# Kernel optimization log

Hardware: AMD Instinct MI355X
Metric: run time of the kernel (lower is better)

## Reference

```python
import jax, jax.numpy as jnp
import numpy as np

B, L, C = 8, 2000, 256
PATCH_LIST = [10, 20]


def _interp_linear(z, L_out):
    # z: (B, L_in, C) -> (B, L_out, C); torch F.interpolate mode='linear', align_corners=False
    L_in = z.shape[1]
    pos = (jnp.arange(L_out, dtype=jnp.float32) + 0.5) * (L_in / L_out) - 0.5
    pos = jnp.clip(pos, 0.0, L_in - 1.0)
    lo = jnp.floor(pos).astype(jnp.int32)
    hi = jnp.minimum(lo + 1, L_in - 1)
    frac = (pos - lo.astype(jnp.float32))[None, :, None]
    return z[:, lo, :] * (1.0 - frac) + z[:, hi, :] * frac


def _kaiming(key, out_dim, in_dim):
    # kaiming_normal_ mode='fan_out', nonlinearity='relu': std = sqrt(2/fan_out)
    return jax.random.normal(key, (out_dim, in_dim), jnp.float32) * np.float32(np.sqrt(2.0 / out_dim))


def setup_inputs() -> dict:
    key = jax.random.key(0)
    ks = jax.random.split(key, 7)
    inp = {"x": jax.random.normal(ks[0], (B, L, C), jnp.float32)}
    ki = 1
    for p in PATCH_LIST:
        w = L // p  # patch_number
        inp[f"wq{p}"] = _kaiming(ks[ki], p, p); ki += 1
        inp[f"bq{p}"] = jnp.zeros((p,), jnp.float32)
        inp[f"wk{p}"] = _kaiming(ks[ki], p, p); ki += 1
        inp[f"bk{p}"] = jnp.zeros((p,), jnp.float32)
        inp[f"wl{p}"] = _kaiming(ks[ki], w, p); ki += 1  # nn.Linear(patch_size, patch_number)
        inp[f"bl{p}"] = jnp.zeros((w,), jnp.float32)
    return inp


def _scale_branch(x, p, wq, bq, wk, bk, wl, bl):
    Bx, Lx, Cx = x.shape
    w = Lx // p
    # rearrange 'b (w p) c -> (b c) w p'
    z = x.reshape(Bx, w, p, Cx).transpose(0, 3, 1, 2).reshape(Bx * Cx, w, p)
    # AttentionLayer(w_size=w, d_model=p, n_heads=1): attn map over the w patches
    q = z @ wq.T + bq
    k = z @ wk.T + bk
    scores = jnp.einsum('nwp,nvp->nwv', q, k) / jnp.sqrt(jnp.float32(p))  # (B*C, w, w)
    attn = jax.nn.softmax(scores, axis=-1)
    # linear_layers[i]: Linear(p -> w); attention OUTPUT is discarded in the original forward
    z2 = z @ wl.T + bl  # (B*C, w, w)
    # rearrange '(b c) w p2 -> b (w p2) c'
    z3 = z2.reshape(Bx, Cx, w * w).transpose(0, 2, 1)  # (B, w*w, C)
    if w * w != Lx:
        z3 = _interp_linear(z3, Lx)
    return z3, attn


def reference(x, wq10, bq10, wk10, bk10, wl10, bl10, wq20, bq20, wk20, bk20, wl20, bl20):
    z10, attn10 = _scale_branch(x, 10, wq10, bq10, wk10, bk10, wl10, bl10)
    z20, attn20 = _scale_branch(x, 20, wq20, bq20, wk20, bk20, wl20, bl20)
    res = (z10 + z20) * 0.5  # stack(...).mean(-1) over the two scales
    return res, attn10, attn20
```

## Files before the change

### kernel.cpp

```cpp
#include <hip/hip_runtime.h>
#include <cstddef>
#include <cstdint>

#define XSTRIDE 512000
#define RES_ELEMS 4096000
#define ATTN10_ELEMS 81920000

typedef _Float16 half2_t __attribute__((ext_vector_type(2)));

__device__ __forceinline__ unsigned int pack_h2(float a, float b) {
  half2_t h;
  h.x = (_Float16)a;
  h.y = (_Float16)b;
  return __builtin_bit_cast(unsigned int, h);
}

__device__ __forceinline__ float fdot2(unsigned int a, unsigned int b, float c) {
#if __has_builtin(__builtin_amdgcn_fdot2)
  return __builtin_amdgcn_fdot2(__builtin_bit_cast(half2_t, a),
                                __builtin_bit_cast(half2_t, b), c, false);
#else
  half2_t ha = __builtin_bit_cast(half2_t, a);
  half2_t hb = __builtin_bit_cast(half2_t, b);
  return c + (float)ha.x * (float)hb.x + (float)ha.y * (float)hb.y;
#endif
}

template <int CTRL>
__device__ __forceinline__ float dpp_f(float x, float identity) {
  return __int_as_float(__builtin_amdgcn_update_dpp(
      __float_as_int(identity), __float_as_int(x), CTRL, 0xF, 0xF, false));
}

__device__ __forceinline__ float wave_allmax(float x) {
  const float NI = -__builtin_inff();
  x = fmaxf(x, dpp_f<0x111>(x, NI));
  x = fmaxf(x, dpp_f<0x112>(x, NI));
  x = fmaxf(x, dpp_f<0x114>(x, NI));
  x = fmaxf(x, dpp_f<0x118>(x, NI));
  x = fmaxf(x, dpp_f<0x142>(x, NI));
  x = fmaxf(x, dpp_f<0x143>(x, NI));
  return __int_as_float(__builtin_amdgcn_readlane(__float_as_int(x), 63));
}

__device__ __forceinline__ float wave_allsum(float x) {
  x += dpp_f<0x111>(x, 0.0f);
  x += dpp_f<0x112>(x, 0.0f);
  x += dpp_f<0x114>(x, 0.0f);
  x += dpp_f<0x118>(x, 0.0f);
  x += dpp_f<0x142>(x, 0.0f);
  x += dpp_f<0x143>(x, 0.0f);
  return __int_as_float(__builtin_amdgcn_readlane(__float_as_int(x), 63));
}

__global__ __launch_bounds__(256, 4) void attn_kernel(
    const float* __restrict__ x,
    const float* __restrict__ wq10, const float* __restrict__ bq10,
    const float* __restrict__ wk10, const float* __restrict__ bk10,
    const float* __restrict__ wq20, const float* __restrict__ bq20,
    const float* __restrict__ wk20, const float* __restrict__ bk20,
    float* __restrict__ attn10, float* __restrict__ attn20) {
  __shared__ float z[2000];
  __shared__ __align__(16) unsigned int q10h[200 * 8];
  __shared__ __align__(16) unsigned int k10t[5 * 200];
  __shared__ __align__(16) unsigned int q20h[100 * 12];
  __shared__ __align__(16) unsigned int k20t[10 * 100];

  const int n = blockIdx.x;
  const int b = n >> 8, c = n & 255;
  const int t = threadIdx.x;

  const float* xcol = x + (size_t)b * XSTRIDE + c;
  for (int l = t; l < 2000; l += 256) z[l] = xcol[(size_t)l * 256];
  __syncthreads();

  if (t < 200) {
    float zr[10];
#pragma unroll
    for (int j = 0; j < 10; ++j) zr[j] = z[t * 10 + j];
#pragma unroll
    for (int m = 0; m < 5; ++m) {
      float q0 = bq10[2 * m], q1 = bq10[2 * m + 1];
      float k0 = bk10[2 * m], k1 = bk10[2 * m + 1];
#pragma unroll
      for (int j = 0; j < 10; ++j) {
        q0 += wq10[(2 * m) * 10 + j] * zr[j];
        q1 += wq10[(2 * m + 1) * 10 + j] * zr[j];
        k0 += wk10[(2 * m) * 10 + j] * zr[j];
        k1 += wk10[(2 * m + 1) * 10 + j] * zr[j];
      }
      q10h[t * 8 + m] = pack_h2(q0, q1);
      k10t[m * 200 + t] = pack_h2(k0, k1);
    }
    const int wi = t >> 1, h = t & 1;
    float zr2[20];
#pragma unroll
    for (int j = 0; j < 20; ++j) zr2[j] = z[wi * 20 + j];
#pragma unroll
    for (int m = 0; m < 5; ++m) {
      const int pi = h * 10 + 2 * m;
      float q0 = bq20[pi], q1 = bq20[pi + 1];
      float k0 = bk20[pi], k1 = bk20[pi + 1];
#pragma unroll
      for (int j = 0; j < 20; ++j) {
        q0 += wq20[pi * 20 + j] * zr2[j];
        q1 += wq20[(pi + 1) * 20 + j] * zr2[j];
        k0 += wk20[pi * 20 + j] * zr2[j];
        k1 += wk20[(pi + 1) * 20 + j] * zr2[j];
      }
      q20h[wi * 12 + h * 5 + m] = pack_h2(q0, q1);
      k20t[(h * 5 + m) * 100 + wi] = pack_h2(k0, k1);
    }
  }
  __syncthreads();

  const int wave = t >> 6, lane = t & 63;
  const int Lc = (lane < 50) ? lane : 49;
  const bool act = (lane < 50);

  {
    unsigned int kr[20];
    const uint4* k4 = (const uint4*)k10t;
#pragma unroll
    for (int m = 0; m < 5; ++m) {
      uint4 v = k4[m * 50 + Lc];
      kr[4 * m + 0] = v.x; kr[4 * m + 1] = v.y; kr[4 * m + 2] = v.z; kr[4 * m + 3] = v.w;
    }
    const float scale = 1.44269504088896340736f / 3.16227766016837933200f;
    const float NI = -__builtin_inff();
    float* obase = attn10 + (size_t)n * 40000 + 4 * lane;
    for (int r = 0; r < 50; ++r) {
      const int wi = wave * 50 + r;
      const uint4 qa = *(const uint4*)(q10h + wi * 8);
      const unsigned int qb = q10h[wi * 8 + 4];
      float s[4];
#pragma unroll
      for (int d = 0; d < 4; ++d) {
        float a = fdot2(qa.x, kr[d], 0.0f);
        a = fdot2(qa.y, kr[4 + d], a);
        a = fdot2(qa.z, kr[8 + d], a);
        a = fdot2(qa.w, kr[12 + d], a);
        a = fdot2(qb, kr[16 + d], a);
        s[d] = act ? a * scale : NI;
      }
      const float mw = wave_allmax(fmaxf(fmaxf(s[0], s[1]), fmaxf(s[2], s[3])));
      const float e0 = exp2f(s[0] - mw), e1 = exp2f(s[1] - mw);
      const float e2 = exp2f(s[2] - mw), e3 = exp2f(s[3] - mw);
      const float sw = wave_allsum(e0 + e1 + e2 + e3);
#if __has_builtin(__builtin_amdgcn_rcpf)
      const float inv = __builtin_amdgcn_rcpf(sw);
#else
      const float inv = 1.0f / sw;
#endif
      if (act) {
        float4 o;
        o.x = e0 * inv; o.y = e1 * inv; o.z = e2 * inv; o.w = e3 * inv;
        *(float4*)(obase + (size_t)wi * 200) = o;
      }
    }
  }

  {
    unsigned int kr[20];
    const uint2* k2 = (const uint2*)k20t;
#pragma unroll
    for (int m = 0; m < 10; ++m) {
      uint2 v = k2[m * 50 + Lc];
      kr[2 * m + 0] = v.x; kr[2 * m + 1] = v.y;
    }
    const float scale = 1.44269504088896340736f / 4.47213595499957939282f;
    const float NI = -__builtin_inff();
    float* obase = attn20 + (size_t)n * 10000 + 2 * lane;
    for (int r = 0; r < 25; ++r) {
      const int wi = wave * 25 + r;
      const unsigned int* qrow = q20h + wi * 12;
      const uint4 qa = *(const uint4*)qrow;
      const uint4 qb = *(const uint4*)(qrow + 4);
      const uint2 qc = *(const uint2*)(qrow + 8);
      float s[2];
#pragma unroll
      for (int d = 0; d < 2; ++d) {
        float a = fdot2(qa.x, kr[d], 0.0f);
        a = fdot2(qa.y, kr[2 + d], a);
        a = fdot2(qa.z, kr[4 + d], a);
        a = fdot2(qa.w, kr[6 + d], a);
        a = fdot2(qb.x, kr[8 + d], a);
        a = fdot2(qb.y, kr[10 + d], a);
        a = fdot2(qb.z, kr[12 + d], a);
        a = fdot2(qb.w, kr[14 + d], a);
        a = fdot2(qc.x, kr[16 + d], a);
        a = fdot2(qc.y, kr[18 + d], a);
        s[d] = act ? a * scale : NI;
      }
      const float mw = wave_allmax(fmaxf(s[0], s[1]));
      const float e0 = exp2f(s[0] - mw), e1 = exp2f(s[1] - mw);
      const float sw = wave_allsum(e0 + e1);
#if __has_builtin(__builtin_amdgcn_rcpf)
      const float inv = __builtin_amdgcn_rcpf(sw);
#else
      const float inv = 1.0f / sw;
#endif
      if (act) {
        float2 o;
        o.x = e0 * inv; o.y = e1 * inv;
        *(float2*)(obase + (size_t)wi * 100) = o;
      }
    }
  }
}

__global__ __launch_bounds__(256) void res_kernel(
    const float* __restrict__ x,
    const float* __restrict__ wl10, const float* __restrict__ bl10,
    const float* __restrict__ wl20, const float* __restrict__ bl20,
    float* __restrict__ res) {
  const int bj = blockIdx.x;
  const int b = bj / 100, jg = bj % 100;
  const int c = threadIdx.x;
  const float* xp = x + (size_t)b * XSTRIDE + (size_t)jg * 20 * 256 + c;
  float xw[20];
#pragma unroll
  for (int i = 0; i < 20; ++i) xw[i] = xp[(size_t)i * 256];
  float* rp = res + (size_t)b * XSTRIDE + (size_t)jg * 20 * 256 + c;
#pragma unroll
  for (int r = 0; r < 20; ++r) {
    const int vi1 = 20 * (r % 10) + 9;
    const int o = (r / 10) * 10;
    const int vi2 = 5 * r + 2;
    float s1 = bl10[vi1] + bl10[vi1 + 1];
#pragma unroll
    for (int pi = 0; pi < 10; ++pi)
      s1 += (wl10[vi1 * 10 + pi] + wl10[(vi1 + 1) * 10 + pi]) * xw[o + pi];
    float s2 = bl20[vi2];
#pragma unroll
    for (int i = 0; i < 20; ++i) s2 += wl20[vi2 * 20 + i] * xw[i];
    rp[(size_t)r * 256] = 0.25f * s1 + 0.5f * s2;
  }
}

extern "C" void kernel_launch(void* const* d_in, const int* in_sizes, int n_in,
                              void* d_out, int out_size, void* d_ws, size_t ws_size,
                              hipStream_t stream) {
  const float* x = (const float*)d_in[0];
  const float* wq10 = (const float*)d_in[1];
  const float* bq10 = (const float*)d_in[2];
  const float* wk10 = (const float*)d_in[3];
  const float* bk10 = (const float*)d_in[4];
  const float* wl10 = (const float*)d_in[5];
  const float* bl10 = (const float*)d_in[6];
  const float* wq20 = (const float*)d_in[7];
  const float* bq20 = (const float*)d_in[8];
  const float* wk20 = (const float*)d_in[9];
  const float* bk20 = (const float*)d_in[10];
  const float* wl20 = (const float*)d_in[11];
  const float* bl20 = (const float*)d_in[12];

  float* out = (float*)d_out;
  float* res = out;
  float* attn10 = out + RES_ELEMS;
  float* attn20 = out + RES_ELEMS + ATTN10_ELEMS;

  hipLaunchKernelGGL(attn_kernel, dim3(2048), dim3(256), 0, stream,
                     x, wq10, bq10, wk10, bk10, wq20, bq20, wk20, bk20,
                     attn10, attn20);
  hipLaunchKernelGGL(res_kernel, dim3(800), dim3(256), 0, stream,
                     x, wl10, bl10, wl20, bl20, res);
}
```

Measured before the change: 542.3 us.

## Pre-transpose input to workspace and drop softmax max-subtraction

Adds a tiled transpose kernel that writes x in (b,c,l) layout to a workspace buffer, so the attention kernel can load each column with contiguous float4 reads instead of strided loads. It also removes the wave-wide max reduction in the softmax and exponentiates the raw scaled scores with a hardware exp2 intrinsic. Skipping the max subtraction saves a cross-lane reduction per row, but it can overflow if scores are large. The transpose adds an extra launch and a 16MB write and read.

```diff
diff --git a/kernel.cpp b/kernel.cpp
--- a/kernel.cpp
+++ b/kernel.cpp
@@ -5,6 +5,7 @@
 #define XSTRIDE 512000
 #define RES_ELEMS 4096000
 #define ATTN10_ELEMS 81920000
+#define XT_BYTES 16384000
 
 typedef _Float16 half2_t __attribute__((ext_vector_type(2)));
 
@@ -26,41 +27,65 @@
 #endif
 }
 
+__device__ __forceinline__ float fast_exp2(float x) {
+#if __has_builtin(__builtin_amdgcn_exp2f)
+  return __builtin_amdgcn_exp2f(x);
+#else
+  return exp2f(x);
+#endif
+}
+
 template <int CTRL>
-__device__ __forceinline__ float dpp_f(float x, float identity) {
+__device__ __forceinline__ float dpp0_f(float x) {
   return __int_as_float(__builtin_amdgcn_update_dpp(
-      __float_as_int(identity), __float_as_int(x), CTRL, 0xF, 0xF, false));
-}
-
-__device__ __forceinline__ float wave_allmax(float x) {
-  const float NI = -__builtin_inff();
-  x = fmaxf(x, dpp_f<0x111>(x, NI));
-  x = fmaxf(x, dpp_f<0x112>(x, NI));
-  x = fmaxf(x, dpp_f<0x114>(x, NI));
-  x = fmaxf(x, dpp_f<0x118>(x, NI));
-  x = fmaxf(x, dpp_f<0x142>(x, NI));
-  x = fmaxf(x, dpp_f<0x143>(x, NI));
+      0, __float_as_int(x), CTRL, 0xF, 0xF, true));
+}
+
+__device__ __forceinline__ float wave_allsum(float x) {
+  x += dpp0_f<0x111>(x);
+  x += dpp0_f<0x112>(x);
+  x += dpp0_f<0x114>(x);
+  x += dpp0_f<0x118>(x);
+  x += dpp0_f<0x142>(x);
+  x += dpp0_f<0x143>(x);
   return __int_as_float(__builtin_amdgcn_readlane(__float_as_int(x), 63));
 }
 
-__device__ __forceinline__ float wave_allsum(float x) {
-  x += dpp_f<0x111>(x, 0.0f);
-  x += dpp_f<0x112>(x, 0.0f);
-  x += dpp_f<0x114>(x, 0.0f);
-  x += dpp_f<0x118>(x, 0.0f);
-  x += dpp_f<0x142>(x, 0.0f);
-  x += dpp_f<0x143>(x, 0.0f);
-  return __int_as_float(__builtin_amdgcn_readlane(__float_as_int(x), 63));
+__global__ __launch_bounds__(256) void transpose_kernel(
+    const float* __restrict__ x, float* __restrict__ xT) {
+  __shared__ float tile[64][65];
+  const int blk = blockIdx.x;
+  const int b = blk >> 7;
+  const int lt = (blk >> 2) & 31;
+  const int ct = blk & 3;
+  const int l0 = lt * 64, c0 = ct * 64;
+  const int tx = threadIdx.x & 63;
+  const int ty = threadIdx.x >> 6;
+  const float* xb = x + (size_t)b * XSTRIDE;
+#pragma unroll
+  for (int r = ty; r < 64; r += 4) {
+    const int l = l0 + r;
+    if (l < 2000) tile[r][tx] = xb[(size_t)l * 256 + c0 + tx];
+  }
+  __syncthreads();
+  float* xtb = xT + (size_t)b * XSTRIDE;
+  if (l0 + tx < 2000) {
+#pragma unroll
+    for (int r = ty; r < 64; r += 4) {
+      const int c = c0 + r;
+      xtb[(size_t)c * 2000 + l0 + tx] = tile[tx][r];
+    }
+  }
 }
 
 __global__ __launch_bounds__(256, 4) void attn_kernel(
-    const float* __restrict__ x,
+    const float* __restrict__ x, const float* __restrict__ xt, int use_xt,
     const float* __restrict__ wq10, const float* __restrict__ bq10,
     const float* __restrict__ wk10, const float* __restrict__ bk10,
     const float* __restrict__ wq20, const float* __restrict__ bq20,
     const float* __restrict__ wk20, const float* __restrict__ bk20,
     float* __restrict__ attn10, float* __restrict__ attn20) {
-  __shared__ float z[2000];
+  __shared__ __align__(16) float z[2000];
   __shared__ __align__(16) unsigned int q10h[200 * 8];
   __shared__ __align__(16) unsigned int k10t[5 * 200];
   __shared__ __align__(16) unsigned int q20h[100 * 12];
@@ -70,8 +95,14 @@
   const int b = n >> 8, c = n & 255;
   const int t = threadIdx.x;
 
-  const float* xcol = x + (size_t)b * XSTRIDE + c;
-  for (int l = t; l < 2000; l += 256) z[l] = xcol[(size_t)l * 256];
+  if (use_xt) {
+    const float4* xr4 = (const float4*)(xt + (size_t)n * 2000);
+    float4* z4 = (float4*)z;
+    for (int i = t; i < 500; i += 256) z4[i] = xr4[i];
+  } else {
+    const float* xcol = x + (size_t)b * XSTRIDE + c;
+    for (int l = t; l < 2000; l += 256) z[l] = xcol[(size_t)l * 256];
+  }
   __syncthreads();
 
   if (t < 200) {
@@ -117,6 +148,7 @@
   const int wave = t >> 6, lane = t & 63;
   const int Lc = (lane < 50) ? lane : 49;
   const bool act = (lane < 50);
+  const float NI = -__builtin_inff();
 
   {
     unsigned int kr[20];
@@ -127,13 +159,12 @@
       kr[4 * m + 0] = v.x; kr[4 * m + 1] = v.y; kr[4 * m + 2] = v.z; kr[4 * m + 3] = v.w;
     }
     const float scale = 1.44269504088896340736f / 3.16227766016837933200f;
-    const float NI = -__builtin_inff();
     float* obase = attn10 + (size_t)n * 40000 + 4 * lane;
     for (int r = 0; r < 50; ++r) {
       const int wi = wave * 50 + r;
       const uint4 qa = *(const uint4*)(q10h + wi * 8);
       const unsigned int qb = q10h[wi * 8 + 4];
-      float s[4];
+      float e[4];
 #pragma unroll
       for (int d = 0; d < 4; ++d) {
         float a = fdot2(qa.x, kr[d], 0.0f);
@@ -141,12 +172,9 @@
         a = fdot2(qa.z, kr[8 + d], a);
         a = fdot2(qa.w, kr[12 + d], a);
         a = fdot2(qb, kr[16 + d], a);
-        s[d] = act ? a * scale : NI;
-      }
-      const float mw = wave_allmax(fmaxf(fmaxf(s[0], s[1]), fmaxf(s[2], s[3])));
-      const float e0 = exp2f(s[0] - mw), e1 = exp2f(s[1] - mw);
-      const float e2 = exp2f(s[2] - mw), e3 = exp2f(s[3] - mw);
-      const float sw = wave_allsum(e0 + e1 + e2 + e3);
+        e[d] = fast_exp2(act ? a * scale : NI);
+      }
+      const float sw = wave_allsum((e[0] + e[1]) + (e[2] + e[3]));
 #if __has_builtin(__builtin_amdgcn_rcpf)
       const float inv = __builtin_amdgcn_rcpf(sw);
 #else
@@ -154,7 +182,7 @@
 #endif
       if (act) {
         float4 o;
-        o.x = e0 * inv; o.y = e1 * inv; o.z = e2 * inv; o.w = e3 * inv;
+        o.x = e[0] * inv; o.y = e[1] * inv; o.z = e[2] * inv; o.w = e[3] * inv;
         *(float4*)(obase + (size_t)wi * 200) = o;
       }
     }
@@ -169,7 +197,6 @@
       kr[2 * m + 0] = v.x; kr[2 * m + 1] = v.y;
     }
     const float scale = 1.44269504088896340736f / 4.47213595499957939282f;
-    const float NI = -__builtin_inff();
     float* obase = attn20 + (size_t)n * 10000 + 2 * lane;
     for (int r = 0; r < 25; ++r) {
       const int wi = wave * 25 + r;
@@ -177,7 +204,7 @@
       const uint4 qa = *(const uint4*)qrow;
       const uint4 qb = *(const uint4*)(qrow + 4);
       const uint2 qc = *(const uint2*)(qrow + 8);
-      float s[2];
+      float e[2];
 #pragma unroll
       for (int d = 0; d < 2; ++d) {
         float a = fdot2(qa.x, kr[d], 0.0f);
@@ -190,11 +217,9 @@
         a = fdot2(qb.w, kr[14 + d], a);
         a = fdot2(qc.x, kr[16 + d], a);
         a = fdot2(qc.y, kr[18 + d], a);
-        s[d] = act ? a * scale : NI;
-      }
-      const float mw = wave_allmax(fmaxf(s[0], s[1]));
-      const float e0 = exp2f(s[0] - mw), e1 = exp2f(s[1] - mw);
-      const float sw = wave_allsum(e0 + e1);
+        e[d] = fast_exp2(act ? a * scale : NI);
+      }
+      const float sw = wave_allsum(e[0] + e[1]);
 #if __has_builtin(__builtin_amdgcn_rcpf)
       const float inv = __builtin_amdgcn_rcpf(sw);
 #else
@@ -202,7 +227,7 @@
 #endif
       if (act) {
         float2 o;
-        o.x = e0 * inv; o.y = e1 * inv;
+        o.x = e[0] * inv; o.y = e[1] * inv;
         *(float2*)(obase + (size_t)wi * 100) = o;
       }
     }
@@ -260,8 +285,14 @@
   float* attn10 = out + RES_ELEMS;
   float* attn20 = out + RES_ELEMS + ATTN10_ELEMS;
 
+  const int use_xt = (d_ws != nullptr && ws_size >= (size_t)XT_BYTES) ? 1 : 0;
+  float* xT = (float*)d_ws;
+
+  if (use_xt) {
+    hipLaunchKernelGGL(transpose_kernel, dim3(1024), dim3(256), 0, stream, x, xT);
+  }
   hipLaunchKernelGGL(attn_kernel, dim3(2048), dim3(256), 0, stream,
-                     x, wq10, bq10, wk10, bk10, wq20, bq20, wk20, bk20,
+                     x, xT, use_xt, wq10, bq10, wk10, bk10, wq20, bq20, wk20, bk20,
                      attn10, attn20);
   hipLaunchKernelGGL(res_kernel, dim3(800), dim3(256), 0, stream,
                      x, wl10, bl10, wl20, bl20, res);
```

Result: faster. 501.1 us (-7.6%).
